# Kernel optimization log

Hardware: AMD Instinct MI355X
Metric: run time of the kernel (lower is better)

Reference implementation:

```python
import jax, jax.numpy as jnp
import numpy as np

B, S, E, H = 4, 1024, 1024, 16

def setup_inputs() -> dict:
    key = jax.random.key(0)
    ks = jax.random.split(key, 7)
    sc = 0.02
    return {
        "queries": jax.random.normal(ks[0], (B, S, E), jnp.float32),
        "keys": jax.random.normal(ks[1], (B, S, E), jnp.float32),
        "values": jax.random.normal(ks[2], (B, S, E), jnp.float32),
        "Wq_w": jax.random.normal(ks[3], (E, E), jnp.float32) * sc,
        "Wq_b": jax.random.normal(ks[4], (E,), jnp.float32) * sc,
        "Wo_w": jax.random.normal(ks[5], (E, E), jnp.float32) * sc,
        "Wo_b": jax.random.normal(ks[6], (E,), jnp.float32) * sc,
        "num_heads": H,
    }

def reference(queries, keys, values, Wq_w, Wq_b, Wo_w, Wo_b, num_heads):
    b, s, e = queries.shape
    dh = e // num_heads

    def proj_heads(x):
        # NOTE: original module applies Wq to q, k AND v (bug kept faithfully)
        y = x @ Wq_w.T + Wq_b                      # [b, s, e]
        return y.reshape(b, s, num_heads, dh)      # [b, s, h, dh]

    q = proj_heads(queries)
    k = proj_heads(keys)
    v = proj_heads(values)

    scores = jnp.einsum('bqhd,bkhd->bhqk', q, k) / jnp.sqrt(jnp.asarray(dh, q.dtype))
    attn = jax.nn.softmax(scores, axis=-1)         # [b, h, q, k]
    out = jnp.einsum('bhqk,bkhd->bqhd', attn, v)   # [b, s, h, dh]
    out = out.reshape(b, s, e)
    return out @ Wo_w.T + Wo_b
```

## Files before the change

kernel.cpp:

```cpp
#include <hip/hip_runtime.h>
#include <stdint.h>


typedef __attribute__((ext_vector_type(8))) short bf16x8;
typedef __attribute__((ext_vector_type(4))) float f32x4;
typedef __attribute__((ext_vector_type(4))) short short4v;

#define GLOAD_LDS(gp, lp)                                                      \
  __builtin_amdgcn_global_load_lds(                                            \
      (__attribute__((address_space(1))) void*)(gp),                           \
      (__attribute__((address_space(3))) void*)(lp), 16, 0, 0)

__device__ __forceinline__ unsigned short f2bf(float f) {
  union { float f; unsigned u; } v; v.f = f;
  unsigned r = v.u + 0x7FFFu + ((v.u >> 16) & 1u);
  return (unsigned short)(r >> 16);
}

template<int SHIFT>
__global__ void cvt3_kernel(const float* __restrict__ s0, const float* __restrict__ s1,
                            const float* __restrict__ s2, short* __restrict__ dst) {
  int i = blockIdx.x * blockDim.x + threadIdx.x;
  int which = i >> SHIFT;
  int j = i & ((1 << SHIFT) - 1);
  const float* src = (which == 0) ? s0 : (which == 1) ? s1 : s2;
  float4 f = reinterpret_cast<const float4*>(src)[j];
  short4v o;
  o.x = (short)f2bf(f.x); o.y = (short)f2bf(f.y);
  o.z = (short)f2bf(f.z); o.w = (short)f2bf(f.w);
  reinterpret_cast<short4v*>(dst)[i] = o;
}

template<int EPI>
__global__ __launch_bounds__(256, 2)
void gemm_bt(const short* __restrict__ A, const short* __restrict__ Bw,
             const float* __restrict__ bias,
             short* __restrict__ qkv, float* __restrict__ outf)
{
  __shared__ short As[128 * 64];
  __shared__ short Bs[128 * 64];
  const int tid  = threadIdx.x;
  const int lane = tid & 63;
  const int g    = lane >> 4;
  const int r7   = lane & 7;
  const int w    = tid >> 6;
  const int wm   = w >> 1, wn = w & 1;

  const int orig = blockIdx.y * 8 + blockIdx.x;
  const int cpx  = (gridDim.x * gridDim.y) >> 3;
  const int t    = (orig & 7) * cpx + (orig >> 3);
  const int m0   = (t >> 3) * 128, n0 = (t & 7) * 128;

  f32x4 acc[4][4] = {};

  for (int k0 = 0; k0 < 1024; k0 += 64) {
#pragma unroll
    for (int c = 0; c < 4; c++) {
      int L   = c * 256 + tid;
      int row = L >> 3;
      int col = ((L & 7) ^ (row & 7)) * 8;
      GLOAD_LDS(A  + (m0 + row) * 1024 + k0 + col, As + L * 8);
      GLOAD_LDS(Bw + (n0 + row) * 1024 + k0 + col, Bs + L * 8);
    }
    __syncthreads();
#pragma unroll
    for (int kk = 0; kk < 2; kk++) {
      bf16x8 av[4], bv[4];
#pragma unroll
      for (int mi = 0; mi < 4; mi++) {
        int row = wm * 64 + mi * 16 + (lane & 15);
        av[mi] = *(const bf16x8*)&As[row * 64 + (((kk * 4 + g) ^ r7) * 8)];
      }
#pragma unroll
      for (int ni = 0; ni < 4; ni++) {
        int row = wn * 64 + ni * 16 + (lane & 15);
        bv[ni] = *(const bf16x8*)&Bs[row * 64 + (((kk * 4 + g) ^ r7) * 8)];
      }
#pragma unroll
      for (int mi = 0; mi < 4; mi++)
#pragma unroll
        for (int ni = 0; ni < 4; ni++)
          acc[mi][ni] = __builtin_amdgcn_mfma_f32_16x16x32_bf16(av[mi], bv[ni], acc[mi][ni], 0, 0, 0);
    }
    __syncthreads();
  }

  if (EPI == 0) {
    const int inp = m0 >> 12;
#pragma unroll
    for (int mi = 0; mi < 4; mi++) {
#pragma unroll
      for (int ni = 0; ni < 4; ni++) {
        const int coll = n0 + wn * 64 + ni * 16 + (lane & 15);
        const float bv = bias[coll];
        const int rbase = m0 + wm * 64 + mi * 16 + (lane >> 4) * 4;
        const int hh = coll >> 6, d = coll & 63;
        if (inp < 2) {
#pragma unroll
          for (int j = 0; j < 4; j++) {
            int rowl = rbase + j;
            int bb = (rowl >> 10) & 3, s = rowl & 1023;
            qkv[(((inp * 4 + bb) * 16 + hh) * 1024 + s) * 64 + d] =
                (short)f2bf(acc[mi][ni][j] + bv);
          }
        } else {
          int bb = (rbase >> 10) & 3, s0 = rbase & 1023;
          short4v o;
          o.x = (short)f2bf(acc[mi][ni][0] + bv);
          o.y = (short)f2bf(acc[mi][ni][1] + bv);
          o.z = (short)f2bf(acc[mi][ni][2] + bv);
          o.w = (short)f2bf(acc[mi][ni][3] + bv);
          *(short4v*)&qkv[8 * 1024 * 1024 + ((bb * 16 + hh) * 64 + d) * 1024 + s0] = o;
        }
      }
    }
  } else {
#pragma unroll
    for (int mi = 0; mi < 4; mi++) {
#pragma unroll
      for (int ni = 0; ni < 4; ni++) {
        const int coll = n0 + wn * 64 + ni * 16 + (lane & 15);
        const float bv = bias[coll];
        const int rbase = m0 + wm * 64 + mi * 16 + (lane >> 4) * 4;
#pragma unroll
        for (int j = 0; j < 4; j++)
          outf[(rbase + j) * 1024 + coll] = acc[mi][ni][j] + bv;
      }
    }
  }
}

__global__ __launch_bounds__(256, 2)
void attn_kernel(const short* __restrict__ qkv, short* __restrict__ O)
{
  __shared__ short Ks[64 * 64];
  __shared__ short VTs[64 * 64];
  __shared__ short QPs[64 * 64];

  const int tid  = threadIdx.x;
  const int lane = tid & 63;
  const int g    = lane >> 4, r7 = lane & 7;
  const int w    = tid >> 6;

  const int t   = (blockIdx.x & 7) * 128 + (blockIdx.x >> 3);
  const int qt  = t & 15, hh = (t >> 4) & 15, bb = t >> 8;
  const int q0  = qt * 64;

  const short* Qg = qkv + (bb * 16 + hh) * 1024 * 64;
  const short* Kg = qkv + 4 * 1024 * 1024 + (bb * 16 + hh) * 1024 * 64;
  const short* Vg = qkv + 8 * 1024 * 1024 + (bb * 16 + hh) * 64 * 1024;

#pragma unroll
  for (int c = 0; c < 2; c++) {
    int L = c * 256 + tid;
    int row = L >> 3;
    int col = ((L & 7) ^ (row & 7)) * 8;
    GLOAD_LDS(Qg + (q0 + row) * 64 + col, QPs + L * 8);
  }
  __syncthreads();
  bf16x8 qf[2];
  {
    const int qrow = w * 16 + (lane & 15);
    qf[0] = *(const bf16x8*)&QPs[qrow * 64 + ((g ^ r7) * 8)];
    qf[1] = *(const bf16x8*)&QPs[qrow * 64 + (((4 + g) ^ r7) * 8)];
  }

  float m_run[4], l_run[4];
  f32x4 acc_o[4] = {};
#pragma unroll
  for (int j = 0; j < 4; j++) { m_run[j] = -1e30f; l_run[j] = 0.0f; }

  for (int kt = 0; kt < 16; kt++) {
    __syncthreads();
#pragma unroll
    for (int c = 0; c < 2; c++) {
      int L = c * 256 + tid;
      int row = L >> 3;
      int col = ((L & 7) ^ (row & 7)) * 8;
      GLOAD_LDS(Kg + (kt * 64 + row) * 64 + col, Ks + L * 8);
      GLOAD_LDS(Vg + row * 1024 + kt * 64 + col, VTs + L * 8);
    }
    __syncthreads();

    f32x4 sa[4] = {};
#pragma unroll
    for (int kk = 0; kk < 2; kk++) {
#pragma unroll
      for (int ni = 0; ni < 4; ni++) {
        int krow = ni * 16 + (lane & 15);
        bf16x8 kf = *(const bf16x8*)&Ks[krow * 64 + (((kk * 4 + g) ^ r7) * 8)];
        sa[ni] = __builtin_amdgcn_mfma_f32_16x16x32_bf16(qf[kk], kf, sa[ni], 0, 0, 0);
      }
    }
    float mt[4];
#pragma unroll
    for (int j = 0; j < 4; j++)
      mt[j] = fmaxf(fmaxf(sa[0][j], sa[1][j]), fmaxf(sa[2][j], sa[3][j]));
#pragma unroll
    for (int off = 1; off < 16; off <<= 1)
#pragma unroll
      for (int j = 0; j < 4; j++)
        mt[j] = fmaxf(mt[j], __shfl_xor(mt[j], off));
    float alpha[4], rs[4];
#pragma unroll
    for (int j = 0; j < 4; j++) {
      float mn = fmaxf(m_run[j], mt[j] * 0.125f);
      alpha[j] = __expf(m_run[j] - mn);
      m_run[j] = mn;
      rs[j] = 0.0f;
    }
#pragma unroll
    for (int ni = 0; ni < 4; ni++) {
      int col = ni * 16 + (lane & 15);
#pragma unroll
      for (int j = 0; j < 4; j++) {
        int row = w * 16 + g * 4 + j;
        float p = __expf(sa[ni][j] * 0.125f - m_run[j]);
        rs[j] += p;
        QPs[row * 64 + (col ^ ((row & 7) << 3))] = (short)f2bf(p);
      }
    }
#pragma unroll
    for (int off = 1; off < 16; off <<= 1)
#pragma unroll
      for (int j = 0; j < 4; j++)
        rs[j] += __shfl_xor(rs[j], off);
#pragma unroll
    for (int j = 0; j < 4; j++)
      l_run[j] = l_run[j] * alpha[j] + rs[j];
#pragma unroll
    for (int di = 0; di < 4; di++)
#pragma unroll
      for (int j = 0; j < 4; j++)
        acc_o[di][j] *= alpha[j];
#pragma unroll
    for (int kk = 0; kk < 2; kk++) {
      int prow = w * 16 + (lane & 15);
      bf16x8 pf = *(const bf16x8*)&QPs[prow * 64 + (((kk * 4 + g) ^ r7) * 8)];
#pragma unroll
      for (int di = 0; di < 4; di++) {
        int vrow = di * 16 + (lane & 15);
        bf16x8 vf = *(const bf16x8*)&VTs[vrow * 64 + (((kk * 4 + g) ^ r7) * 8)];
        acc_o[di] = __builtin_amdgcn_mfma_f32_16x16x32_bf16(pf, vf, acc_o[di], 0, 0, 0);
      }
    }
  }

#pragma unroll
  for (int di = 0; di < 4; di++) {
    int d = hh * 64 + di * 16 + (lane & 15);
#pragma unroll
    for (int j = 0; j < 4; j++) {
      int q = q0 + w * 16 + g * 4 + j;
      O[(bb * 1024 + q) * 1024 + d] = (short)f2bf(acc_o[di][j] / l_run[j]);
    }
  }
}

extern "C" void kernel_launch(void* const* d_in, const int* in_sizes, int n_in,
                              void* d_out, int out_size, void* d_ws, size_t ws_size,
                              hipStream_t stream)
{
  (void)in_sizes; (void)n_in; (void)out_size; (void)ws_size;
  const float* q    = (const float*)d_in[0];
  const float* k    = (const float*)d_in[1];
  const float* v    = (const float*)d_in[2];
  const float* Wq_w = (const float*)d_in[3];
  const float* Wq_b = (const float*)d_in[4];
  const float* Wo_w = (const float*)d_in[5];
  const float* Wo_b = (const float*)d_in[6];
  float* out = (float*)d_out;

  short* ws   = (short*)d_ws;
  short* Xbf  = ws;
  short* Obf  = ws;
  short* Wqb  = ws + 12582912;
  short* Wob  = ws + 13631488;
  short* qkv  = ws + 14680064;

  cvt3_kernel<20><<<12288, 256, 0, stream>>>(q, k, v, Xbf);
  cvt3_kernel<18><<<2048, 256, 0, stream>>>(Wq_w, Wo_w, Wo_w, Wqb);

  dim3 gp(8, 96);
  gemm_bt<0><<<gp, 256, 0, stream>>>(Xbf, Wqb, Wq_b, qkv, nullptr);

  attn_kernel<<<1024, 256, 0, stream>>>(qkv, Obf);

  dim3 gf(8, 32);
  gemm_bt<1><<<gf, 256, 0, stream>>>(Obf, Wob, Wo_b, nullptr, out);
}
```

Baseline: 210.6 us.

## Double-buffer K/V tiles in attention, use exp2 softmax, merge convert kernels

The attention kernel now keeps two LDS buffers for K and V. It issues the async global-to-LDS loads for the next key tile before computing on the current one, so each iteration needs one barrier instead of two. The softmax folds log2(e) into the scale and calls the hardware exp2 directly instead of __expf. The two fp32-to-bf16 conversion launches become one kernel covering q, k, v, Wq and Wo, which also drops the redundant third weight conversion. The cost is more LDS per block, which could lower occupancy, and the overlap relies on the barrier waiting for the outstanding async loads.

```diff
diff --git a/kernel.cpp b/kernel.cpp
--- a/kernel.cpp
+++ b/kernel.cpp
@@ -17,13 +17,16 @@
   return (unsigned short)(r >> 16);
 }
 
-template<int SHIFT>
-__global__ void cvt3_kernel(const float* __restrict__ s0, const float* __restrict__ s1,
-                            const float* __restrict__ s2, short* __restrict__ dst) {
-  int i = blockIdx.x * blockDim.x + threadIdx.x;
-  int which = i >> SHIFT;
-  int j = i & ((1 << SHIFT) - 1);
-  const float* src = (which == 0) ? s0 : (which == 1) ? s1 : s2;
+__global__ void cvt_all(const float* __restrict__ q, const float* __restrict__ k,
+                        const float* __restrict__ v, const float* __restrict__ wq,
+                        const float* __restrict__ wo, short* __restrict__ dst) {
+  int i = blockIdx.x * 256 + threadIdx.x;
+  const float* src; int j;
+  if (i < 1048576)      { src = q;  j = i; }
+  else if (i < 2097152) { src = k;  j = i - 1048576; }
+  else if (i < 3145728) { src = v;  j = i - 2097152; }
+  else if (i < 3407872) { src = wq; j = i - 3145728; }
+  else                  { src = wo; j = i - 3407872; }
   float4 f = reinterpret_cast<const float4*>(src)[j];
   short4v o;
   o.x = (short)f2bf(f.x); o.y = (short)f2bf(f.y);
@@ -133,8 +136,8 @@
 __global__ __launch_bounds__(256, 2)
 void attn_kernel(const short* __restrict__ qkv, short* __restrict__ O)
 {
-  __shared__ short Ks[64 * 64];
-  __shared__ short VTs[64 * 64];
+  __shared__ short Ks[2][64 * 64];
+  __shared__ short VTs[2][64 * 64];
   __shared__ short QPs[64 * 64];
 
   const int tid  = threadIdx.x;
@@ -156,6 +159,8 @@
     int row = L >> 3;
     int col = ((L & 7) ^ (row & 7)) * 8;
     GLOAD_LDS(Qg + (q0 + row) * 64 + col, QPs + L * 8);
+    GLOAD_LDS(Kg + row * 64 + col,        &Ks[0][L * 8]);
+    GLOAD_LDS(Vg + row * 1024 + col,      &VTs[0][L * 8]);
   }
   __syncthreads();
   bf16x8 qf[2];
@@ -165,22 +170,24 @@
     qf[1] = *(const bf16x8*)&QPs[qrow * 64 + (((4 + g) ^ r7) * 8)];
   }
 
+  const float SC = 0.125f * 1.44269504f;
   float m_run[4], l_run[4];
   f32x4 acc_o[4] = {};
 #pragma unroll
   for (int j = 0; j < 4; j++) { m_run[j] = -1e30f; l_run[j] = 0.0f; }
 
+  int cur = 0;
   for (int kt = 0; kt < 16; kt++) {
-    __syncthreads();
-#pragma unroll
-    for (int c = 0; c < 2; c++) {
-      int L = c * 256 + tid;
-      int row = L >> 3;
-      int col = ((L & 7) ^ (row & 7)) * 8;
-      GLOAD_LDS(Kg + (kt * 64 + row) * 64 + col, Ks + L * 8);
-      GLOAD_LDS(Vg + row * 1024 + kt * 64 + col, VTs + L * 8);
-    }
-    __syncthreads();
+    if (kt < 15) {
+#pragma unroll
+      for (int c = 0; c < 2; c++) {
+        int L = c * 256 + tid;
+        int row = L >> 3;
+        int col = ((L & 7) ^ (row & 7)) * 8;
+        GLOAD_LDS(Kg + ((kt + 1) * 64 + row) * 64 + col, &Ks[cur ^ 1][L * 8]);
+        GLOAD_LDS(Vg + row * 1024 + (kt + 1) * 64 + col, &VTs[cur ^ 1][L * 8]);
+      }
+    }
 
     f32x4 sa[4] = {};
 #pragma unroll
@@ -188,7 +195,7 @@
 #pragma unroll
       for (int ni = 0; ni < 4; ni++) {
         int krow = ni * 16 + (lane & 15);
-        bf16x8 kf = *(const bf16x8*)&Ks[krow * 64 + (((kk * 4 + g) ^ r7) * 8)];
+        bf16x8 kf = *(const bf16x8*)&Ks[cur][krow * 64 + (((kk * 4 + g) ^ r7) * 8)];
         sa[ni] = __builtin_amdgcn_mfma_f32_16x16x32_bf16(qf[kk], kf, sa[ni], 0, 0, 0);
       }
     }
@@ -204,8 +211,8 @@
     float alpha[4], rs[4];
 #pragma unroll
     for (int j = 0; j < 4; j++) {
-      float mn = fmaxf(m_run[j], mt[j] * 0.125f);
-      alpha[j] = __expf(m_run[j] - mn);
+      float mn = fmaxf(m_run[j], mt[j] * SC);
+      alpha[j] = __builtin_amdgcn_exp2f(m_run[j] - mn);
       m_run[j] = mn;
       rs[j] = 0.0f;
     }
@@ -215,7 +222,7 @@
 #pragma unroll
       for (int j = 0; j < 4; j++) {
         int row = w * 16 + g * 4 + j;
-        float p = __expf(sa[ni][j] * 0.125f - m_run[j]);
+        float p = __builtin_amdgcn_exp2f(sa[ni][j] * SC - m_run[j]);
         rs[j] += p;
         QPs[row * 64 + (col ^ ((row & 7) << 3))] = (short)f2bf(p);
       }
@@ -240,10 +247,12 @@
 #pragma unroll
       for (int di = 0; di < 4; di++) {
         int vrow = di * 16 + (lane & 15);
-        bf16x8 vf = *(const bf16x8*)&VTs[vrow * 64 + (((kk * 4 + g) ^ r7) * 8)];
+        bf16x8 vf = *(const bf16x8*)&VTs[cur][vrow * 64 + (((kk * 4 + g) ^ r7) * 8)];
         acc_o[di] = __builtin_amdgcn_mfma_f32_16x16x32_bf16(pf, vf, acc_o[di], 0, 0, 0);
       }
     }
+    __syncthreads();
+    cur ^= 1;
   }
 
 #pragma unroll
@@ -278,8 +287,7 @@
   short* Wob  = ws + 13631488;
   short* qkv  = ws + 14680064;
 
-  cvt3_kernel<20><<<12288, 256, 0, stream>>>(q, k, v, Xbf);
-  cvt3_kernel<18><<<2048, 256, 0, stream>>>(Wq_w, Wo_w, Wo_w, Wqb);
+  cvt_all<<<14336, 256, 0, stream>>>(q, k, v, Wq_w, Wo_w, ws);
 
   dim3 gp(8, 96);
   gemm_bt<0><<<gp, 256, 0, stream>>>(Xbf, Wqb, Wq_b, qkv, nullptr);
```

Result: no change. 209.3 us (-0.6%).
